# Kernel optimization log

Hardware: AMD Instinct MI355X
Metric: run time of the kernel (lower is better)

## Reference

```python
import jax, jax.numpy as jnp
import numpy as np

HG, WG, DG = 16, 16, 8   # bilateral grid size
NP = 12                  # affine params per pixel (3x4)
DS = 256                 # input_downsample


def _resize_bilinear(x, oh, ow):
    # torch F.interpolate(mode='bilinear', align_corners=False)
    B, C, H, W = x.shape
    sy, sx = H / oh, W / ow
    ys = jnp.clip((jnp.arange(oh, dtype=x.dtype) + 0.5) * sy - 0.5, 0.0, H - 1)
    xs = jnp.clip((jnp.arange(ow, dtype=x.dtype) + 0.5) * sx - 0.5, 0.0, W - 1)
    y0 = jnp.floor(ys).astype(jnp.int32); y1 = jnp.minimum(y0 + 1, H - 1)
    x0 = jnp.floor(xs).astype(jnp.int32); x1 = jnp.minimum(x0 + 1, W - 1)
    wy = (ys - y0.astype(x.dtype))[None, None, :, None]
    wx = (xs - x0.astype(x.dtype))[None, None, None, :]
    top = x[:, :, y0, :] * (1 - wy) + x[:, :, y1, :] * wy      # [B,C,oh,W]
    return top[:, :, :, x0] * (1 - wx) + top[:, :, :, x1] * wx  # [B,C,oh,ow]


def _conv(x, w, b):
    y = jax.lax.conv_general_dilated(x, w, (1, 1), 'SAME',
                                     dimension_numbers=('NCHW', 'OIHW', 'NCHW'))
    return y + b[None, :, None, None]


def _slice(grid, guide):
    # grid [B,C,Hg,Wg,D], guide [B,H,W] in [0,1].
    # Equivalent to the per-depth grid_sample(align_corners=True, border) +
    # depth gather/lerp loop: one fused trilinear lookup per pixel.
    B, C, Hg, Wg, D = grid.shape
    H, W = guide.shape[1], guide.shape[2]
    ys = jnp.arange(H, dtype=grid.dtype) * ((Hg - 1) / (H - 1))
    xs = jnp.arange(W, dtype=grid.dtype) * ((Wg - 1) / (W - 1))
    y0 = jnp.floor(ys).astype(jnp.int32); y1 = jnp.minimum(y0 + 1, Hg - 1)
    x0 = jnp.floor(xs).astype(jnp.int32); x1 = jnp.minimum(x0 + 1, Wg - 1)
    wy = (ys - y0.astype(grid.dtype))[:, None]   # [H,1]
    wx = (xs - x0.astype(grid.dtype))[None, :]   # [1,W]
    d = guide * (D - 1)
    d0 = jnp.clip(jnp.floor(d), 0, D - 1).astype(jnp.int32)
    d1 = jnp.minimum(d0 + 1, D - 1)
    wd = jnp.clip(d - d0.astype(grid.dtype), 0.0, 1.0)  # [B,H,W]

    Y0, Y1 = y0[:, None], y1[:, None]
    X0, X1 = x0[None, :], x1[None, :]

    def per_b(g, d0b, d1b, wdb):
        def dlerp(yi, xi):
            # g[:, yi, xi, d] -> [C,H,W]; lerp over depth
            return (1 - wdb) * g[:, yi, xi, d0b] + wdb * g[:, yi, xi, d1b]
        return ((1 - wy) * (1 - wx) * dlerp(Y0, X0)
                + (1 - wy) * wx * dlerp(Y0, X1)
                + wy * (1 - wx) * dlerp(Y1, X0)
                + wy * wx * dlerp(Y1, X1))

    return jax.vmap(per_b)(grid, d0, d1, wd)  # [B,C,H,W]


def _forward(x, w1, b1, w2, b2, w3, b3, w4, b4, w5, b5, w6, b6):
    B, C, H, W = x.shape
    guide = jnp.clip(0.299 * x[:, 0] + 0.587 * x[:, 1] + 0.114 * x[:, 2], 0.0, 1.0)
    scale = min(1.0, DS / max(H, W))
    if scale < 1.0:
        x_low = _resize_bilinear(x, int(H * scale), int(W * scale))
    else:
        x_low = x
    f = jax.nn.relu(_conv(x_low, w1, b1))
    f = jax.nn.relu(_conv(f, w2, b2))
    f = jax.nn.relu(_conv(f, w3, b3))
    c = jax.nn.relu(_conv(f, w4, b4))
    c = jax.nn.relu(_conv(c, w5, b5))
    c = _conv(c, w6, b6)                        # [B, NP*DG, H_low, W_low]
    c = _resize_bilinear(c, HG, WG)             # [B, NP*DG, HG, WG]
    grid = c.reshape(B, NP, DG, HG, WG).transpose(0, 1, 3, 4, 2)  # [B,NP,HG,WG,DG]
    sc = _slice(grid, guide)                    # [B, NP, H, W]
    co = sc.reshape(B, 3, 4, H, W)
    y = jnp.einsum('bijhw,bjhw->bihw', co[:, :, :3], x) + co[:, :, 3]
    return jnp.clip(y, 0.0, 1.0)


def setup_inputs() -> dict:
    key = jax.random.key(0)
    ks = jax.random.split(key, 7)
    x = jax.random.uniform(ks[0], (2, 3, 1024, 1024), dtype=jnp.float32)
    def wmat(k, o, i):
        return jax.random.normal(k, (o, i, 3, 3), jnp.float32) / np.sqrt(i * 9.0)
    return dict(
        x=x,
        w1=wmat(ks[1], 16, 3), b1=jnp.zeros((16,), jnp.float32),
        w2=wmat(ks[2], 32, 16), b2=jnp.zeros((32,), jnp.float32),
        w3=wmat(ks[3], 32, 32), b3=jnp.zeros((32,), jnp.float32),
        w4=wmat(ks[4], 64, 32), b4=jnp.zeros((64,), jnp.float32),
        w5=wmat(ks[5], 64, 64), b5=jnp.zeros((64,), jnp.float32),
        w6=wmat(ks[6], 96, 64), b6=jnp.zeros((96,), jnp.float32),
    )


def reference(x, w1, b1, w2, b2, w3, b3, w4, b4, w5, b5, w6, b6):
    return _forward(x, w1, b1, w2, b2, w3, b3, w4, b4, w5, b5, w6, b6)
```

## Files before the change

kernel.cpp:

```cpp
#include <hip/hip_runtime.h>
#include <hip/hip_bf16.h>

#define HW1K  1048576

typedef float  f4    __attribute__((ext_vector_type(4)));
typedef float  f32x4 __attribute__((ext_vector_type(4)));
typedef short  s16x8 __attribute__((ext_vector_type(8)));
typedef unsigned short u16x8 __attribute__((ext_vector_type(8)));

__device__ __forceinline__ float bf2f(unsigned short u) {
    unsigned int b = ((unsigned int)u) << 16;
    return __builtin_bit_cast(float, b);
}
__device__ __forceinline__ void fsplit(float x, unsigned short& h, unsigned short& l) {
    unsigned int xb = __builtin_bit_cast(unsigned int, x);
    h = (unsigned short)(xb >> 16);
    float fh = __builtin_bit_cast(float, xb & 0xffff0000u);
    float r = x - fh;
    l = (unsigned short)(__builtin_bit_cast(unsigned int, r) >> 16);
}

__global__ __launch_bounds__(256)
void prep_wM(const float* __restrict__ w2, const float* __restrict__ w3,
             const float* __restrict__ w4, const float* __restrict__ w5,
             const float* __restrict__ w6,
             unsigned short* __restrict__ Wh, unsigned short* __restrict__ Wl) {
    int i = blockIdx.x * 256 + threadIdx.x;
    if (i >= 124928) return;
    const float* src; int base, cin, kp_;
    if      (i < 5120)  { src = w2; base = 0;     cin = 16; kp_ = 160; }
    else if (i < 14336) { src = w3; base = 5120;  cin = 32; kp_ = 288; }
    else if (i < 32768) { src = w4; base = 14336; cin = 32; kp_ = 288; }
    else if (i < 69632) { src = w5; base = 32768; cin = 64; kp_ = 576; }
    else                { src = w6; base = 69632; cin = 64; kp_ = 576; }
    int r  = i - base;
    int co = r / kp_;
    int kp = r % kp_;
    int kk = kp / cin;
    int ci = kp % cin;
    float v = (kk < 9) ? src[(co * cin + ci) * 9 + kk] : 0.0f;
    unsigned short h, l; fsplit(v, h, l);
    Wh[i] = h; Wl[i] = l;
}

template <int WIN, int CIN, int COUT, int KP, int SO, int HOIST>
__device__ __forceinline__ void layerM(const unsigned short* sH, const unsigned short* sL,
                                       unsigned short* dH, unsigned short* dL,
                                       const unsigned short* __restrict__ Wh,
                                       const unsigned short* __restrict__ Wl,
                                       const float* __restrict__ bias) {
    constexpr int WOUT = WIN - 2;
    constexpr int NPX  = WOUT * WOUT;
    constexpr int CINP = CIN + 8;
    constexpr int MT   = (NPX + 15) / 16;
    constexpr int NT   = COUT / 16;
    constexpr int WPN  = 8 / NT;
    constexpr int KS   = KP / 32;

    const int wid  = threadIdx.x >> 6;
    const int lane = threadIdx.x & 63;
    const int m    = lane & 15;
    const int g    = lane >> 4;

    const int nt    = wid % NT;
    const int chunk = wid / NT;
    const int co    = nt * 16 + m;

    const unsigned short* wbh = Wh + (size_t)co * KP + 8 * g;
    const unsigned short* wbl = Wl + (size_t)co * KP + 8 * g;

    s16x8 bH[HOIST ? KS : 1], bL[HOIST ? KS : 1];
    if constexpr (HOIST) {
        #pragma unroll
        for (int k0 = 0; k0 < KS; ++k0) {
            bH[k0] = *(const s16x8*)(wbh + k0 * 32);
            bL[k0] = *(const s16x8*)(wbl + k0 * 32);
        }
    }
    const float bv = bias[co];

    #pragma unroll 1
    for (int mt = chunk; mt < MT; mt += WPN) {
        const int mt0 = mt * 16;
        int px = mt0 + m; if (px > NPX - 1) px = NPX - 1;
        const int pbase = (px / WOUT) * WIN + (px % WOUT);

        f32x4 aHH = {0,0,0,0}, aHL = {0,0,0,0}, aLH = {0,0,0,0};
        #pragma unroll
        for (int k0 = 0; k0 < KS; ++k0) {
            const int k   = k0 * 32 + 8 * g;
            const int kk  = k / CIN;
            const int ci0 = k % CIN;
            const int aoff = (pbase + (kk / 3) * WIN + (kk % 3)) * CINP + ci0;
            s16x8 avh = *(const s16x8*)(&sH[aoff]);
            s16x8 avl = *(const s16x8*)(&sL[aoff]);
            s16x8 bvh, bvl;
            if constexpr (HOIST) { bvh = bH[k0]; bvl = bL[k0]; }
            else {
                bvh = *(const s16x8*)(wbh + k0 * 32);
                bvl = *(const s16x8*)(wbl + k0 * 32);
            }
            aHH = __builtin_amdgcn_mfma_f32_16x16x32_bf16(avh, bvh, aHH, 0, 0, 0);
            aHL = __builtin_amdgcn_mfma_f32_16x16x32_bf16(avh, bvl, aHL, 0, 0, 0);
            aLH = __builtin_amdgcn_mfma_f32_16x16x32_bf16(avl, bvh, aLH, 0, 0, 0);
        }
        #pragma unroll
        for (int j = 0; j < 4; ++j) {
            int opx = mt0 + g * 4 + j;
            if (opx < NPX) {
                float v = fmaxf(aHH[j] + aHL[j] + aLH[j] + bv, 0.0f);
                unsigned short h, l; fsplit(v, h, l);
                dH[opx * SO + co] = h;
                dL[opx * SO + co] = l;
            }
        }
    }
}

__global__ __launch_bounds__(512, 2)
void fusedM(const float* __restrict__ x, const float* __restrict__ w1,
            const float* __restrict__ b1,
            const unsigned short* __restrict__ Wh, const unsigned short* __restrict__ Wl,
            const float* __restrict__ b2, const float* __restrict__ b3,
            const float* __restrict__ b4, const float* __restrict__ b5,
            unsigned short* __restrict__ P6h, unsigned short* __restrict__ P6l) {
    __shared__ float sC[592];
    __shared__ __align__(16) unsigned short AH[3840], AL[3840];
    __shared__ __align__(16) unsigned short BH[4000], BL[4000];

    const int cell = blockIdx.x;
    const int b = cell >> 8, gy = (cell >> 4) & 15, gx = cell & 15;

    for (int i = threadIdx.x; i < 588; i += 512) {
        int c = i / 196, t = i % 196;
        int xi = t % 14, yi = t / 14;
        int ya = 16 * gy + 1 + yi, xa = 16 * gx + 1 + xi;
        const float* p = x + ((size_t)(b * 3 + c)) * HW1K + (4 * ya + 1) * 1024 + (4 * xa + 1);
        sC[i] = 0.25f * (p[0] + p[1] + p[1024] + p[1025]);
    }
    for (int i = threadIdx.x; i < 384; i += 512) { AH[3456 + i] = 0; AL[3456 + i] = 0; }
    __syncthreads();

    {
        const int wid  = __builtin_amdgcn_readfirstlane(threadIdx.x >> 6);
        const int lane = threadIdx.x & 63;
        const int co0  = (wid & 3) * 4;
        const int s0   = wid >> 2;
        #pragma unroll 1
        for (int s = s0; s < 3; s += 2) {
            int px = lane + s * 64; if (px > 143) px = 143;
            const int pb = (px / 12) * 14 + (px % 12);
            f4 acc;
            #pragma unroll
            for (int j = 0; j < 4; ++j) acc[j] = b1[co0 + j];
            for (int ci = 0; ci < 3; ++ci)
                #pragma unroll
                for (int k = 0; k < 9; ++k) {
                    float w[4];
                    #pragma unroll
                    for (int j = 0; j < 4; ++j) w[j] = w1[((co0 + j) * 3 + ci) * 9 + k];
                    float a = sC[ci * 196 + pb + (k / 3) * 14 + (k % 3)];
                    #pragma unroll
                    for (int j = 0; j < 4; ++j) acc[j] = fmaf(w[j], a, acc[j]);
                }
            #pragma unroll
            for (int j = 0; j < 4; ++j) {
                float v = fmaxf(acc[j], 0.0f);
                unsigned short h, l; fsplit(v, h, l);
                AH[px * 24 + co0 + j] = h;
                AL[px * 24 + co0 + j] = l;
            }
        }
    }
    __syncthreads();

    layerM<12, 16, 32, 160, 40, 1>(AH, AL, BH, BL, Wh + 0,     Wl + 0,     b2);
    __syncthreads();
    layerM<10, 32, 32, 288, 40, 1>(BH, BL, AH, AL, Wh + 5120,  Wl + 5120,  b3);
    __syncthreads();
    layerM< 8, 32, 64, 288, 72, 1>(AH, AL, BH, BL, Wh + 14336, Wl + 14336, b4);
    __syncthreads();
    layerM< 6, 64, 64, 576, 72, 0>(BH, BL, AH, AL, Wh + 32768, Wl + 32768, b5);
    __syncthreads();

    for (int t = threadIdx.x; t < 576; t += 512) {
        int kk = t >> 6, ci = t & 63;
        int ky = kk / 3, kx = kk % 3;
        float v = 0.0f;
        #pragma unroll
        for (int dr = 0; dr < 2; ++dr)
            #pragma unroll
            for (int dc = 0; dc < 2; ++dc) {
                int px = (ky + dr) * 4 + (kx + dc);
                v += bf2f(AH[px * 72 + ci]) + bf2f(AL[px * 72 + ci]);
            }
        v *= 0.25f;
        unsigned short h, l; fsplit(v, h, l);
        P6h[(size_t)cell * 576 + t] = h;
        P6l[(size_t)cell * 576 + t] = l;
    }
}

__global__ __launch_bounds__(64)
void gemm6(const unsigned short* __restrict__ Bh, const unsigned short* __restrict__ Bl,
           const unsigned short* __restrict__ W6h, const unsigned short* __restrict__ W6l,
           const float* __restrict__ b6, float* __restrict__ c16) {
    const int cell0 = blockIdx.x * 16;
    const int co0   = blockIdx.y * 16;
    const int lane  = threadIdx.x;
    const int m = lane & 15, g = lane >> 4;

    const unsigned short* pah = Bh  + (size_t)(cell0 + m) * 576 + 8 * g;
    const unsigned short* pal = Bl  + (size_t)(cell0 + m) * 576 + 8 * g;
    const unsigned short* pbh = W6h + (size_t)(co0 + m) * 576 + 8 * g;
    const unsigned short* pbl = W6l + (size_t)(co0 + m) * 576 + 8 * g;

    f32x4 aHH = {0,0,0,0}, aHL = {0,0,0,0}, aLH = {0,0,0,0};
    #pragma unroll 6
    for (int k0 = 0; k0 < 576; k0 += 32) {
        s16x8 avh = *(const s16x8*)(pah + k0);
        s16x8 avl = *(const s16x8*)(pal + k0);
        s16x8 bvh = *(const s16x8*)(pbh + k0);
        s16x8 bvl = *(const s16x8*)(pbl + k0);
        aHH = __builtin_amdgcn_mfma_f32_16x16x32_bf16(avh, bvh, aHH, 0, 0, 0);
        aHL = __builtin_amdgcn_mfma_f32_16x16x32_bf16(avh, bvl, aHL, 0, 0, 0);
        aLH = __builtin_amdgcn_mfma_f32_16x16x32_bf16(avl, bvh, aLH, 0, 0, 0);
    }
    const int co = co0 + m;
    const float bv = b6[co];
    #pragma unroll
    for (int j = 0; j < 4; ++j) {
        int cell = cell0 + g * 4 + j;
        float v = aHH[j] + aHL[j] + aLH[j] + bv;
        int b = cell >> 8, gyx = cell & 255;
        c16[(size_t)b * 24576 + (gyx * 8 + (co & 7)) * 12 + (co >> 3)] = v;
    }
}

__global__ __launch_bounds__(256)
void slice_apply4(const float* __restrict__ x, const float* __restrict__ c16,
                  float* __restrict__ out) {
    int t = blockIdx.x * 256 + threadIdx.x;
    int po4 = t * 4;
    int b   = po4 >> 20;
    int po  = po4 & (HW1K - 1);
    int py  = po >> 10;
    int px0 = po & 1023;

    const float* xb = x + (size_t)b * 3 * HW1K;
    f4 rv  = *(const f4*)(xb + po);
    f4 gv  = *(const f4*)(xb + HW1K + po);
    f4 bv  = *(const f4*)(xb + 2 * HW1K + po);

    float ysf = (float)py * (15.0f / 1023.0f);
    int y0 = (int)floorf(ysf); int y1 = min(y0 + 1, 15);
    float wy = ysf - (float)y0;

    const float* gb = c16 + (size_t)b * 24576;
    f4 outv[3];

    #pragma unroll
    for (int s = 0; s < 4; ++s) {
        float r  = rv[s], g = gv[s], bl = bv[s];
        int   px = px0 + s;

        float gd = fminf(fmaxf(0.299f * r + 0.587f * g + 0.114f * bl, 0.0f), 1.0f);

        float xsf = (float)px * (15.0f / 1023.0f);
        int x0 = (int)floorf(xsf); int x1 = min(x0 + 1, 15);
        float wx = xsf - (float)x0;

        float d  = gd * 7.0f;
        int d0 = (int)floorf(d); d0 = max(0, min(d0, 7));
        int d1 = min(d0 + 1, 7);
        float wd = fminf(fmaxf(d - (float)d0, 0.0f), 1.0f);

        float co[12];
        #pragma unroll
        for (int p = 0; p < 12; ++p) co[p] = 0.0f;

        #pragma unroll
        for (int cy = 0; cy < 2; ++cy) {
            int   yy  = cy ? y1 : y0;
            float wyf = cy ? wy : 1.0f - wy;
            #pragma unroll
            for (int cx = 0; cx < 2; ++cx) {
                int   xx  = cx ? x1 : x0;
                float wyx = wyf * (cx ? wx : 1.0f - wx);
                const float* g0 = gb + ((yy * 16 + xx) * 8 + d0) * 12;
                const float* g1 = gb + ((yy * 16 + xx) * 8 + d1) * 12;
                float wA = wyx * (1.0f - wd), wB = wyx * wd;
                #pragma unroll
                for (int p = 0; p < 12; ++p) co[p] += wA * g0[p] + wB * g1[p];
            }
        }

        #pragma unroll
        for (int i = 0; i < 3; ++i) {
            float v = co[i * 4 + 0] * r + co[i * 4 + 1] * g + co[i * 4 + 2] * bl + co[i * 4 + 3];
            outv[i][s] = fminf(fmaxf(v, 0.0f), 1.0f);
        }
    }

    float* ob = out + (size_t)b * 3 * HW1K;
    #pragma unroll
    for (int i = 0; i < 3; ++i)
        *(f4*)(ob + i * HW1K + po) = outv[i];
}

extern "C" void kernel_launch(void* const* d_in, const int* in_sizes, int n_in,
                              void* d_out, int out_size, void* d_ws, size_t ws_size,
                              hipStream_t stream) {
    const float* x  = (const float*)d_in[0];
    const float* w1 = (const float*)d_in[1];  const float* b1 = (const float*)d_in[2];
    const float* w2 = (const float*)d_in[3];  const float* b2 = (const float*)d_in[4];
    const float* w3 = (const float*)d_in[5];  const float* b3 = (const float*)d_in[6];
    const float* w4 = (const float*)d_in[7];  const float* b4 = (const float*)d_in[8];
    const float* w5 = (const float*)d_in[9];  const float* b5 = (const float*)d_in[10];
    const float* w6 = (const float*)d_in[11]; const float* b6 = (const float*)d_in[12];
    float* out = (float*)d_out;

    char* w = (char*)d_ws;
    unsigned short* Wh  = (unsigned short*)w;   w += 124928 * 2;
    unsigned short* Wl  = (unsigned short*)w;   w += 124928 * 2;
    unsigned short* P6h = (unsigned short*)w;   w += 512 * 576 * 2;
    unsigned short* P6l = (unsigned short*)w;   w += 512 * 576 * 2;
    float*          c16 = (float*)w;

    prep_wM<<<dim3(489),  dim3(256), 0, stream>>>(w2, w3, w4, w5, w6, Wh, Wl);
    fusedM <<<dim3(512),  dim3(512), 0, stream>>>(x, w1, b1, Wh, Wl, b2, b3, b4, b5, P6h, P6l);
    gemm6  <<<dim3(32, 6), dim3(64), 0, stream>>>(P6h, P6l, Wh + 69632, Wl + 69632, b6, c16);
    slice_apply4<<<dim3(2 * HW1K / 4 / 256), dim3(256), 0, stream>>>(x, c16, out);

    (void)in_sizes; (void)n_in; (void)out_size; (void)ws_size;
}
```

Before: 71.73 us.

## Run fused conv stack with one wavefront per cell, dropping block barriers

The fused per-cell conv kernel now runs with a single 64-lane wavefront per block instead of 512 threads. Each lane loops over all output-channel tiles and pixel tiles itself, so the __syncthreads barriers between layers go away. Layer 1 loads the 27 input taps into registers once and reuses them for every output-channel group. The trade-off is about 8x less parallelism per cell: only 512 wavefronts cover the whole GPU, with serialized MFMA work and higher register pressure from hoisting all weights in every layer, including the 576-wide layer 5.

New measurement: 104.4 us. +45.5%, slower.

```diff
diff --git a/kernel.cpp b/kernel.cpp
--- a/kernel.cpp
+++ b/kernel.cpp
@@ -43,8 +43,8 @@
     Wh[i] = h; Wl[i] = l;
 }
 
-template <int WIN, int CIN, int COUT, int KP, int SO, int HOIST>
-__device__ __forceinline__ void layerM(const unsigned short* sH, const unsigned short* sL,
+template <int WIN, int CIN, int COUT, int KP, int SO>
+__device__ __forceinline__ void layerW(const unsigned short* sH, const unsigned short* sL,
                                        unsigned short* dH, unsigned short* dL,
                                        const unsigned short* __restrict__ Wh,
                                        const unsigned short* __restrict__ Wl,
@@ -54,71 +54,61 @@
     constexpr int CINP = CIN + 8;
     constexpr int MT   = (NPX + 15) / 16;
     constexpr int NT   = COUT / 16;
-    constexpr int WPN  = 8 / NT;
     constexpr int KS   = KP / 32;
 
-    const int wid  = threadIdx.x >> 6;
-    const int lane = threadIdx.x & 63;
+    const int lane = threadIdx.x;
     const int m    = lane & 15;
     const int g    = lane >> 4;
 
-    const int nt    = wid % NT;
-    const int chunk = wid / NT;
-    const int co    = nt * 16 + m;
-
-    const unsigned short* wbh = Wh + (size_t)co * KP + 8 * g;
-    const unsigned short* wbl = Wl + (size_t)co * KP + 8 * g;
-
-    s16x8 bH[HOIST ? KS : 1], bL[HOIST ? KS : 1];
-    if constexpr (HOIST) {
+    #pragma unroll 1
+    for (int nt = 0; nt < NT; ++nt) {
+        const int co = nt * 16 + m;
+        const unsigned short* wbh = Wh + (size_t)co * KP + 8 * g;
+        const unsigned short* wbl = Wl + (size_t)co * KP + 8 * g;
+
+        s16x8 bH[KS], bL[KS];
         #pragma unroll
         for (int k0 = 0; k0 < KS; ++k0) {
             bH[k0] = *(const s16x8*)(wbh + k0 * 32);
             bL[k0] = *(const s16x8*)(wbl + k0 * 32);
         }
-    }
-    const float bv = bias[co];
-
-    #pragma unroll 1
-    for (int mt = chunk; mt < MT; mt += WPN) {
-        const int mt0 = mt * 16;
-        int px = mt0 + m; if (px > NPX - 1) px = NPX - 1;
-        const int pbase = (px / WOUT) * WIN + (px % WOUT);
-
-        f32x4 aHH = {0,0,0,0}, aHL = {0,0,0,0}, aLH = {0,0,0,0};
-        #pragma unroll
-        for (int k0 = 0; k0 < KS; ++k0) {
-            const int k   = k0 * 32 + 8 * g;
-            const int kk  = k / CIN;
-            const int ci0 = k % CIN;
-            const int aoff = (pbase + (kk / 3) * WIN + (kk % 3)) * CINP + ci0;
-            s16x8 avh = *(const s16x8*)(&sH[aoff]);
-            s16x8 avl = *(const s16x8*)(&sL[aoff]);
-            s16x8 bvh, bvl;
-            if constexpr (HOIST) { bvh = bH[k0]; bvl = bL[k0]; }
-            else {
-                bvh = *(const s16x8*)(wbh + k0 * 32);
-                bvl = *(const s16x8*)(wbl + k0 * 32);
-            }
-            aHH = __builtin_amdgcn_mfma_f32_16x16x32_bf16(avh, bvh, aHH, 0, 0, 0);
-            aHL = __builtin_amdgcn_mfma_f32_16x16x32_bf16(avh, bvl, aHL, 0, 0, 0);
-            aLH = __builtin_amdgcn_mfma_f32_16x16x32_bf16(avl, bvh, aLH, 0, 0, 0);
-        }
-        #pragma unroll
-        for (int j = 0; j < 4; ++j) {
-            int opx = mt0 + g * 4 + j;
-            if (opx < NPX) {
-                float v = fmaxf(aHH[j] + aHL[j] + aLH[j] + bv, 0.0f);
-                unsigned short h, l; fsplit(v, h, l);
-                dH[opx * SO + co] = h;
-                dL[opx * SO + co] = l;
-            }
-        }
-    }
-}
-
-__global__ __launch_bounds__(512, 2)
-void fusedM(const float* __restrict__ x, const float* __restrict__ w1,
+        const float bv = bias[co];
+
+        #pragma unroll 1
+        for (int mt = 0; mt < MT; ++mt) {
+            const int mt0 = mt * 16;
+            int px = mt0 + m; if (px > NPX - 1) px = NPX - 1;
+            const int pbase = (px / WOUT) * WIN + (px % WOUT);
+
+            f32x4 aHH = {0,0,0,0}, aHL = {0,0,0,0}, aLH = {0,0,0,0};
+            #pragma unroll
+            for (int k0 = 0; k0 < KS; ++k0) {
+                const int k   = k0 * 32 + 8 * g;
+                const int kk  = k / CIN;
+                const int ci0 = k % CIN;
+                const int aoff = (pbase + (kk / 3) * WIN + (kk % 3)) * CINP + ci0;
+                s16x8 avh = *(const s16x8*)(&sH[aoff]);
+                s16x8 avl = *(const s16x8*)(&sL[aoff]);
+                aHH = __builtin_amdgcn_mfma_f32_16x16x32_bf16(avh, bH[k0], aHH, 0, 0, 0);
+                aHL = __builtin_amdgcn_mfma_f32_16x16x32_bf16(avh, bL[k0], aHL, 0, 0, 0);
+                aLH = __builtin_amdgcn_mfma_f32_16x16x32_bf16(avl, bH[k0], aLH, 0, 0, 0);
+            }
+            #pragma unroll
+            for (int j = 0; j < 4; ++j) {
+                int opx = mt0 + g * 4 + j;
+                if (opx < NPX) {
+                    float v = fmaxf(aHH[j] + aHL[j] + aLH[j] + bv, 0.0f);
+                    unsigned short h, l; fsplit(v, h, l);
+                    dH[opx * SO + co] = h;
+                    dL[opx * SO + co] = l;
+                }
+            }
+        }
+    }
+}
+
+__global__ __launch_bounds__(64, 1)
+void fusedW(const float* __restrict__ x, const float* __restrict__ w1,
             const float* __restrict__ b1,
             const unsigned short* __restrict__ Wh, const unsigned short* __restrict__ Wl,
             const float* __restrict__ b2, const float* __restrict__ b3,
@@ -130,38 +120,40 @@
 
     const int cell = blockIdx.x;
     const int b = cell >> 8, gy = (cell >> 4) & 15, gx = cell & 15;
-
-    for (int i = threadIdx.x; i < 588; i += 512) {
+    const int lane = threadIdx.x;
+
+    for (int i = lane; i < 588; i += 64) {
         int c = i / 196, t = i % 196;
         int xi = t % 14, yi = t / 14;
         int ya = 16 * gy + 1 + yi, xa = 16 * gx + 1 + xi;
         const float* p = x + ((size_t)(b * 3 + c)) * HW1K + (4 * ya + 1) * 1024 + (4 * xa + 1);
         sC[i] = 0.25f * (p[0] + p[1] + p[1024] + p[1025]);
     }
-    for (int i = threadIdx.x; i < 384; i += 512) { AH[3456 + i] = 0; AL[3456 + i] = 0; }
-    __syncthreads();
-
-    {
-        const int wid  = __builtin_amdgcn_readfirstlane(threadIdx.x >> 6);
-        const int lane = threadIdx.x & 63;
-        const int co0  = (wid & 3) * 4;
-        const int s0   = wid >> 2;
+    for (int i = lane; i < 384; i += 64) { AH[3456 + i] = 0; AL[3456 + i] = 0; }
+
+    #pragma unroll 1
+    for (int s = 0; s < 3; ++s) {
+        int px = lane + s * 64; if (px > 143) px = 143;
+        const int pb = (px / 12) * 14 + (px % 12);
+        float a[27];
+        #pragma unroll
+        for (int ci = 0; ci < 3; ++ci)
+            #pragma unroll
+            for (int k = 0; k < 9; ++k)
+                a[ci * 9 + k] = sC[ci * 196 + pb + (k / 3) * 14 + (k % 3)];
         #pragma unroll 1
-        for (int s = s0; s < 3; s += 2) {
-            int px = lane + s * 64; if (px > 143) px = 143;
-            const int pb = (px / 12) * 14 + (px % 12);
+        for (int c4 = 0; c4 < 4; ++c4) {
+            const int co0 = c4 * 4;
             f4 acc;
             #pragma unroll
             for (int j = 0; j < 4; ++j) acc[j] = b1[co0 + j];
+            #pragma unroll
             for (int ci = 0; ci < 3; ++ci)
                 #pragma unroll
                 for (int k = 0; k < 9; ++k) {
-                    float w[4];
                     #pragma unroll
-                    for (int j = 0; j < 4; ++j) w[j] = w1[((co0 + j) * 3 + ci) * 9 + k];
-                    float a = sC[ci * 196 + pb + (k / 3) * 14 + (k % 3)];
-                    #pragma unroll
-                    for (int j = 0; j < 4; ++j) acc[j] = fmaf(w[j], a, acc[j]);
+                    for (int j = 0; j < 4; ++j)
+                        acc[j] = fmaf(w1[((co0 + j) * 3 + ci) * 9 + k], a[ci * 9 + k], acc[j]);
                 }
             #pragma unroll
             for (int j = 0; j < 4; ++j) {
@@ -172,18 +164,13 @@
             }
         }
     }
-    __syncthreads();
-
-    layerM<12, 16, 32, 160, 40, 1>(AH, AL, BH, BL, Wh + 0,     Wl + 0,     b2);
-    __syncthreads();
-    layerM<10, 32, 32, 288, 40, 1>(BH, BL, AH, AL, Wh + 5120,  Wl + 5120,  b3);
-    __syncthreads();
-    layerM< 8, 32, 64, 288, 72, 1>(AH, AL, BH, BL, Wh + 14336, Wl + 14336, b4);
-    __syncthreads();
-    layerM< 6, 64, 64, 576, 72, 0>(BH, BL, AH, AL, Wh + 32768, Wl + 32768, b5);
-    __syncthreads();
-
-    for (int t = threadIdx.x; t < 576; t += 512) {
+
+    layerW<12, 16, 32, 160, 40>(AH, AL, BH, BL, Wh + 0,     Wl + 0,     b2);
+    layerW<10, 32, 32, 288, 40>(BH, BL, AH, AL, Wh + 5120,  Wl + 5120,  b3);
+    layerW< 8, 32, 64, 288, 72>(AH, AL, BH, BL, Wh + 14336, Wl + 14336, b4);
+    layerW< 6, 64, 64, 576, 72>(BH, BL, AH, AL, Wh + 32768, Wl + 32768, b5);
+
+    for (int t = lane; t < 576; t += 64) {
         int kk = t >> 6, ci = t & 63;
         int ky = kk / 3, kx = kk % 3;
         float v = 0.0f;
@@ -328,7 +315,7 @@
     float*          c16 = (float*)w;
 
     prep_wM<<<dim3(489),  dim3(256), 0, stream>>>(w2, w3, w4, w5, w6, Wh, Wl);
-    fusedM <<<dim3(512),  dim3(512), 0, stream>>>(x, w1, b1, Wh, Wl, b2, b3, b4, b5, P6h, P6l);
+    fusedW <<<dim3(512),  dim3(64),  0, stream>>>(x, w1, b1, Wh, Wl, b2, b3, b4, b5, P6h, P6l);
     gemm6  <<<dim3(32, 6), dim3(64), 0, stream>>>(P6h, P6l, Wh + 69632, Wl + 69632, b6, c16);
     slice_apply4<<<dim3(2 * HW1K / 4 / 256), dim3(256), 0, stream>>>(x, c16, out);
 
```
